# Optimization experiments

Hardware: AMD Instinct MI355X
Metric: run time of the kernel (lower is better)

## Reference

```python
import jax, jax.numpy as jnp
import numpy as np

NUM_EXPERTS = 8


def setup_inputs() -> dict:
    key = jax.random.key(0)
    k1, k2, k3 = jax.random.split(key, 3)
    M, K, E, N, TOPK = 16384, 1024, NUM_EXPERTS, 2048, 2
    local_hidden_states = jax.random.normal(k1, (M, K), dtype=jnp.float32)
    up_weight = jax.random.normal(k2, (E, K, N), dtype=jnp.float32) * 0.02
    full_topk_ids = jax.random.randint(k3, (M, TOPK), 0, E, dtype=jnp.int64)
    return {
        "local_hidden_states": local_hidden_states,
        "up_weight": up_weight,
        "full_topk_ids": full_topk_ids,
    }


def reference(local_hidden_states, up_weight, full_topk_ids):
    # WORLD_SIZE == 1 -> all-gather is the identity; full token set == local shard.
    full_hidden = local_hidden_states                     # [M, K]
    M, K = full_hidden.shape
    E, _, N = up_weight.shape
    topk = full_topk_ids.shape[1]

    # Each token is routed to `topk` experts: replicate rows, flatten routing ids.
    h_rep = jnp.repeat(full_hidden, topk, axis=0)         # [M*topk, K]
    flat_ids = full_topk_ids.reshape(-1)                  # [M*topk]

    # Expert-grouped GEMM: out[p] = h_rep[p] @ up_weight[flat_ids[p]].
    # Loop over the small fixed expert count, masking rows (dense reference
    # for the irregular grouped GEMM; avoids a [M*topk, K, N] weight gather).
    inter = jnp.zeros((M * topk, N), dtype=full_hidden.dtype)
    for e in range(E):
        mask = (flat_ids == e).astype(full_hidden.dtype)[:, None]   # [M*topk, 1]
        inter = inter + (h_rep @ up_weight[e]) * mask                # [M*topk, N]

    # Fused gated SiLU: split the fused gate/up projection in half.
    half = N // 2
    gate, up = inter[:, :half], inter[:, half:]
    return jax.nn.silu(gate) * up                          # [M*topk, N//2]
```

## Files before the change

kernel.cpp:

```cpp
#include <hip/hip_runtime.h>
#include <hip/hip_bf16.h>
#include <stdint.h>

typedef __attribute__((ext_vector_type(4))) float f32x4;
typedef __attribute__((ext_vector_type(8))) short bf16x8;
typedef __attribute__((ext_vector_type(4))) float float4v;

static constexpr int KD    = 1024;
static constexpr int ND    = 2048;
static constexpr int NE    = 8;
static constexpr int MROWS = 16384;
static constexpr int RFLAT = 32768;
static constexpr int OUTN  = 1024;

static constexpr size_t WS_ROWLIST = 1024;
static constexpr size_t WS_HB      = 262144;
static constexpr size_t WS_WT      = 262144 + (size_t)33554432;

__device__ __forceinline__ unsigned short f2bf(float f) {
  uint32_t u = __float_as_uint(f);
  uint32_t r = (u + 0x7FFFu + ((u >> 16) & 1u)) >> 16;
  return (unsigned short)r;
}

__device__ __forceinline__ void gload16(const void* g, void* l) {
  __builtin_amdgcn_global_load_lds(
      (__attribute__((address_space(1))) void*)(void*)g,
      (__attribute__((address_space(3))) void*)l, 16, 0, 0);
}

__global__ void k_detect(const int* __restrict__ ids32, int* __restrict__ wsi) {
  int t = blockIdx.x * 256 + threadIdx.x;
  int i = 2 * t + 1;
  if (i < RFLAT && ids32[i] != 0) atomicOr(&wsi[31], 1);
}

__device__ __forceinline__ int read_id(const int* ids32, int t, int mode) {
  return (mode ? ids32[t] : ids32[2 * t]) & 7;
}

__global__ void k_count(const int* __restrict__ ids, int* __restrict__ wsi) {
  __shared__ int h[8];
  const int tid = threadIdx.x;
  if (tid < 8) h[tid] = 0;
  __syncthreads();
  const int mode = wsi[31];
  const int base = blockIdx.x * 512 + tid;
  atomicAdd(&h[read_id(ids, base, mode)], 1);
  atomicAdd(&h[read_id(ids, base + 256, mode)], 1);
  __syncthreads();
  if (tid < 8 && h[tid]) atomicAdd(&wsi[tid], h[tid]);
}

__global__ void k_scan(int* wsi) {
  if (threadIdx.x == 0) {
    int o = 0, to = 0;
    for (int e = 0; e < NE; ++e) {
      int c = wsi[e];
      wsi[16 + e] = o;
      wsi[8 + e]  = o;
      wsi[40 + e] = to;
      o += c;
      to += (c + 255) / 256;
    }
    wsi[16 + NE] = o;
    wsi[40 + NE] = to;
  }
}

__global__ void k_scatter(const int* __restrict__ ids, int* __restrict__ wsi,
                          int* __restrict__ rowlist) {
  __shared__ int h[8], base[8], c2[8];
  const int tid = threadIdx.x;
  if (tid < 8) { h[tid] = 0; c2[tid] = 0; }
  __syncthreads();
  const int mode = wsi[31];
  const int t = blockIdx.x * 256 + tid;
  const int e = read_id(ids, t, mode);
  atomicAdd(&h[e], 1);
  __syncthreads();
  if (tid < 8 && h[tid]) base[tid] = atomicAdd(&wsi[8 + tid], h[tid]);
  __syncthreads();
  const int r = atomicAdd(&c2[e], 1);
  rowlist[base[e] + r] = t;
}

__global__ void k_cvtH(const float* __restrict__ H, unsigned short* __restrict__ Hb) {
  const int n4 = (MROWS * KD) / 4;
  const int stride = gridDim.x * blockDim.x;
  for (int i = blockIdx.x * blockDim.x + threadIdx.x; i < n4; i += stride) {
    float4v v = ((const float4v*)H)[i];
    ushort4 o;
    o.x = f2bf(v.x); o.y = f2bf(v.y); o.z = f2bf(v.z); o.w = f2bf(v.w);
    ((ushort4*)Hb)[i] = o;
  }
}

__global__ void k_cvtW(const float* __restrict__ W, unsigned short* __restrict__ Wt) {
  __shared__ float tile[64][65];
  const int e  = blockIdx.z;
  const int n0 = blockIdx.x * 64;
  const int k0 = blockIdx.y * 64;
  const int tx = threadIdx.x, ty = threadIdx.y;
  const float* Wp = W + (size_t)e * KD * ND;
  #pragma unroll
  for (int i = ty; i < 64; i += 8)
    tile[i][tx] = Wp[(size_t)(k0 + i) * ND + n0 + tx];
  __syncthreads();
  unsigned short* Wo = Wt + (size_t)e * ND * KD;
  #pragma unroll
  for (int i = ty; i < 64; i += 8)
    Wo[(size_t)(n0 + i) * KD + k0 + tx] = f2bf(tile[tx][i]);
}

__global__ __launch_bounds__(512, 2) void k_gemm(
    const unsigned short* __restrict__ Hb, const unsigned short* __restrict__ Wt,
    const int* __restrict__ wsi, const int* __restrict__ rowlist,
    float* __restrict__ Out) {
  const int bid = blockIdx.x;
  const int xcd = bid & 7;
  const int j   = bid >> 3;
  const int colblk = j & 7;
  const int rt  = xcd + (j >> 3) * 8;
  if (rt >= wsi[48]) return;
  int e = 0;
  #pragma unroll
  for (int q = 1; q < 8; ++q)
    if (rt >= wsi[40 + q]) e = q;
  const int cnt = wsi[e];
  const int tile_base = (rt - wsi[40 + e]) * 256;
  const int tile_cnt = min(256, cnt - tile_base);
  const int off = wsi[16 + e] + tile_base;
  const int c0 = colblk * 128;

  __shared__ char lds[131072];
  __shared__ int s_rows[256];

  const int t = threadIdx.x;
  if (t < 256) s_rows[t] = rowlist[off + min(t, tile_cnt - 1)];
  __syncthreads();

  const int srow = t >> 2;
  const int g16 = ((t & 3) ^ ((t >> 3) & 3)) * 16;
  const char* srcA[2];
  const char* srcB[2];
  #pragma unroll
  for (int u = 0; u < 2; ++u) {
    const int row_a = u * 128 + srow;
    srcA[u] = (const char*)Hb + (size_t)(s_rows[row_a] >> 1) * (KD * 2) + g16;
    const int jb = u * 128 + srow;
    const int wn_s = jb >> 6, r64 = jb & 63;
    const int h_s = r64 >> 4, l_s = r64 & 15;
    const int wcol = (h_s < 2) ? (c0 + wn_s * 32 + h_s * 16 + l_s)
                               : (OUTN + c0 + wn_s * 32 + (h_s - 2) * 16 + l_s);
    srcB[u] = (const char*)Wt + ((size_t)e * ND + wcol) * (KD * 2) + g16;
  }

  const int lane = t & 63, wid = t >> 6;
  const int wm = wid >> 2, wn = wid & 3;
  const int kc = lane >> 4, l15 = lane & 15;

  f32x4 acc[8][4];
  #pragma unroll
  for (int m = 0; m < 8; ++m)
    #pragma unroll
    for (int h = 0; h < 4; ++h)
      acc[m][h] = (f32x4){0.f, 0.f, 0.f, 0.f};

  int aoff[8], boff[4];
  #pragma unroll
  for (int m = 0; m < 8; ++m) {
    const int r = wm * 128 + m * 16 + l15;
    aoff[m] = r * 64 + (kc ^ ((r >> 1) & 3)) * 16;
  }
  #pragma unroll
  for (int h = 0; h < 4; ++h) {
    const int jb = wn * 64 + h * 16 + l15;
    boff[h] = 16384 + jb * 64 + (kc ^ ((jb >> 1) & 3)) * 16;
  }

  auto STAGE = [&](int kt, int b) {
    const int go = kt * 64;
    char* base = lds + b * 32768 + t * 16;
    gload16(srcA[0] + go, base);
    gload16(srcA[1] + go, base + 8192);
    gload16(srcB[0] + go, base + 16384);
    gload16(srcB[1] + go, base + 24576);
  };
  auto COMPUTE = [&](int b) {
    const char* cb = lds + b * 32768;
    bf16x8 af[8], bfv[4];
    #pragma unroll
    for (int m = 0; m < 8; ++m) af[m] = *(const bf16x8*)(cb + aoff[m]);
    #pragma unroll
    for (int h = 0; h < 4; ++h) bfv[h] = *(const bf16x8*)(cb + boff[h]);
    #pragma unroll
    for (int m = 0; m < 8; ++m)
      #pragma unroll
      for (int h = 0; h < 4; ++h)
        acc[m][h] = __builtin_amdgcn_mfma_f32_16x16x32_bf16(af[m], bfv[h], acc[m][h], 0, 0, 0);
  };

  STAGE(0, 0); STAGE(1, 1); STAGE(2, 2);
  asm volatile("s_waitcnt vmcnt(8)\ns_barrier" ::: "memory");

  for (int k = 0; k < 29; ++k) {
    STAGE(k + 3, (k + 3) & 3);
    COMPUTE(k & 3);
    asm volatile("s_waitcnt vmcnt(8)\ns_barrier" ::: "memory");
  }
  COMPUTE(29 & 3);
  asm volatile("s_waitcnt vmcnt(4)\ns_barrier" ::: "memory");
  COMPUTE(30 & 3);
  asm volatile("s_waitcnt vmcnt(0)\ns_barrier" ::: "memory");
  COMPUTE(31 & 3);

  #pragma unroll
  for (int m = 0; m < 8; ++m) {
    const int rbase = wm * 128 + m * 16 + kc * 4;
    #pragma unroll
    for (int i = 0; i < 4; ++i) {
      const int rl = rbase + i;
      if (rl < tile_cnt) {
        const size_t orow = (size_t)s_rows[rl] * OUTN;
        #pragma unroll
        for (int h = 0; h < 2; ++h) {
          float gg = acc[m][h][i];
          float uu = acc[m][h + 2][i];
          float s = gg / (1.0f + __expf(-gg)) * uu;
          Out[orow + c0 + wn * 32 + h * 16 + l15] = s;
        }
      }
    }
  }
}

extern "C" void kernel_launch(void* const* d_in, const int* in_sizes, int n_in,
                              void* d_out, int out_size, void* d_ws, size_t ws_size,
                              hipStream_t stream) {
  const float* H  = (const float*)d_in[0];
  const float* W  = (const float*)d_in[1];
  const int* ids  = (const int*)d_in[2];
  float* Out      = (float*)d_out;
  char* ws        = (char*)d_ws;
  int* wsi        = (int*)ws;
  int* rowlist    = (int*)(ws + WS_ROWLIST);
  unsigned short* Hb = (unsigned short*)(ws + WS_HB);
  unsigned short* Wt = (unsigned short*)(ws + WS_WT);

  hipMemsetAsync(ws, 0, 1024, stream);
  k_detect<<<RFLAT / 2 / 256, 256, 0, stream>>>(ids, wsi);
  k_count<<<RFLAT / 512, 256, 0, stream>>>(ids, wsi);
  k_scan<<<1, 64, 0, stream>>>(wsi);
  k_scatter<<<RFLAT / 256, 256, 0, stream>>>(ids, wsi, rowlist);
  k_cvtH<<<2048, 256, 0, stream>>>(H, Hb);
  k_cvtW<<<dim3(ND / 64, KD / 64, NE), dim3(64, 8), 0, stream>>>(W, Wt);
  k_gemm<<<8 * 17 * 8, 512, 0, stream>>>(Hb, Wt, wsi, rowlist, Out);
}
```

Baseline: 262.8 us.

## Restructure GEMM main loop into double-buffered 128-K tiles with interleaved phases

Replaces the 4-stage, 64-wide K pipeline with a 2-buffer scheme using 128-wide K tiles split into two 64-wide halves. Each iteration interleaves LDS fragment loads, global-to-LDS prefetches of the next tile, and MFMA groups in four phases, raising wave priority during MFMA with s_setprio. The goal is to overlap memory and matrix work at a finer grain, in a style similar to ping-pong scheduling. In exchange it adds many more barriers per iteration and relies on the vmcnt waits being correct for the new load ordering.

```diff
diff --git a/kernel.cpp b/kernel.cpp
--- a/kernel.cpp
+++ b/kernel.cpp
@@ -141,20 +141,17 @@
   __syncthreads();
 
   const int srow = t >> 2;
-  const int g16 = ((t & 3) ^ ((t >> 3) & 3)) * 16;
-  const char* srcA[2];
-  const char* srcB[2];
-  #pragma unroll
-  for (int u = 0; u < 2; ++u) {
-    const int row_a = u * 128 + srow;
-    srcA[u] = (const char*)Hb + (size_t)(s_rows[row_a] >> 1) * (KD * 2) + g16;
-    const int jb = u * 128 + srow;
-    const int wn_s = jb >> 6, r64 = jb & 63;
+  const int coff = ((t & 3) ^ ((t >> 3) & 3)) * 16;
+  const char* sA0 = (const char*)Hb + (size_t)(s_rows[srow] >> 1) * (KD * 2) + coff;
+  const char* sA1 = (const char*)Hb + (size_t)(s_rows[128 + srow] >> 1) * (KD * 2) + coff;
+  auto wcol_of = [&](int jc) {
+    const int wn_s = jc >> 6, r64 = jc & 63;
     const int h_s = r64 >> 4, l_s = r64 & 15;
-    const int wcol = (h_s < 2) ? (c0 + wn_s * 32 + h_s * 16 + l_s)
-                               : (OUTN + c0 + wn_s * 32 + (h_s - 2) * 16 + l_s);
-    srcB[u] = (const char*)Wt + ((size_t)e * ND + wcol) * (KD * 2) + g16;
-  }
+    return (h_s < 2) ? (c0 + wn_s * 32 + h_s * 16 + l_s)
+                     : (OUTN + c0 + wn_s * 32 + (h_s - 2) * 16 + l_s);
+  };
+  const char* sB0 = (const char*)Wt + ((size_t)e * ND + wcol_of(srow)) * (KD * 2) + coff;
+  const char* sB1 = (const char*)Wt + ((size_t)e * ND + wcol_of(128 + srow)) * (KD * 2) + coff;
 
   const int lane = t & 63, wid = t >> 6;
   const int wm = wid >> 2, wn = wid & 3;
@@ -167,53 +164,88 @@
     for (int h = 0; h < 4; ++h)
       acc[m][h] = (f32x4){0.f, 0.f, 0.f, 0.f};
 
-  int aoff[8], boff[4];
-  #pragma unroll
-  for (int m = 0; m < 8; ++m) {
-    const int r = wm * 128 + m * 16 + l15;
-    aoff[m] = r * 64 + (kc ^ ((r >> 1) & 3)) * 16;
-  }
-  #pragma unroll
-  for (int h = 0; h < 4; ++h) {
-    const int jb = wn * 64 + h * 16 + l15;
-    boff[h] = 16384 + jb * 64 + (kc ^ ((jb >> 1) & 3)) * 16;
-  }
-
-  auto STAGE = [&](int kt, int b) {
-    const int go = kt * 64;
-    char* base = lds + b * 32768 + t * 16;
-    gload16(srcA[0] + go, base);
-    gload16(srcA[1] + go, base + 8192);
-    gload16(srcB[0] + go, base + 16384);
-    gload16(srcB[1] + go, base + 24576);
-  };
-  auto COMPUTE = [&](int b) {
-    const char* cb = lds + b * 32768;
-    bf16x8 af[8], bfv[4];
-    #pragma unroll
-    for (int m = 0; m < 8; ++m) af[m] = *(const bf16x8*)(cb + aoff[m]);
-    #pragma unroll
-    for (int h = 0; h < 4; ++h) bfv[h] = *(const bf16x8*)(cb + boff[h]);
-    #pragma unroll
-    for (int m = 0; m < 8; ++m)
+  int aoff[2][8], boff[2][4];
+  #pragma unroll
+  for (int q = 0; q < 2; ++q) {
+    #pragma unroll
+    for (int m = 0; m < 8; ++m) {
+      const int r = wm * 128 + m * 16 + l15;
+      aoff[q][m] = q * 16384 + r * 64 + ((kc ^ ((r >> 1) & 3)) * 16);
+    }
+    #pragma unroll
+    for (int h = 0; h < 4; ++h) {
+      const int jb = wn * 64 + h * 16 + l15;
+      boff[q][h] = 32768 + q * 16384 + jb * 64 + ((kc ^ ((jb >> 1) & 3)) * 16);
+    }
+  }
+
+  auto SA = [&](int kt, int q, char* buf) {
+    const int go = kt * 128 + q * 64;
+    gload16(sA0 + go, buf + q * 16384 + t * 16);
+    gload16(sA1 + go, buf + q * 16384 + 8192 + t * 16);
+  };
+  auto SB = [&](int kt, int q, char* buf) {
+    const int go = kt * 128 + q * 64;
+    gload16(sB0 + go, buf + 32768 + q * 16384 + t * 16);
+    gload16(sB1 + go, buf + 32768 + q * 16384 + 8192 + t * 16);
+  };
+
+  bf16x8 af[4], bfv[4];
+  auto LDA = [&](const char* cb, int q, int mlo) {
+    #pragma unroll
+    for (int m = 0; m < 4; ++m) af[m] = *(const bf16x8*)(cb + aoff[q][mlo + m]);
+  };
+  auto LDB = [&](const char* cb, int q) {
+    #pragma unroll
+    for (int h = 0; h < 4; ++h) bfv[h] = *(const bf16x8*)(cb + boff[q][h]);
+  };
+  auto MM = [&](int mlo) {
+    __builtin_amdgcn_s_setprio(1);
+    #pragma unroll
+    for (int m = 0; m < 4; ++m)
       #pragma unroll
       for (int h = 0; h < 4; ++h)
-        acc[m][h] = __builtin_amdgcn_mfma_f32_16x16x32_bf16(af[m], bfv[h], acc[m][h], 0, 0, 0);
-  };
-
-  STAGE(0, 0); STAGE(1, 1); STAGE(2, 2);
-  asm volatile("s_waitcnt vmcnt(8)\ns_barrier" ::: "memory");
-
-  for (int k = 0; k < 29; ++k) {
-    STAGE(k + 3, (k + 3) & 3);
-    COMPUTE(k & 3);
-    asm volatile("s_waitcnt vmcnt(8)\ns_barrier" ::: "memory");
-  }
-  COMPUTE(29 & 3);
-  asm volatile("s_waitcnt vmcnt(4)\ns_barrier" ::: "memory");
-  COMPUTE(30 & 3);
-  asm volatile("s_waitcnt vmcnt(0)\ns_barrier" ::: "memory");
-  COMPUTE(31 & 3);
+        acc[mlo + m][h] =
+            __builtin_amdgcn_mfma_f32_16x16x32_bf16(af[m], bfv[h], acc[mlo + m][h], 0, 0, 0);
+    __builtin_amdgcn_s_setprio(0);
+  };
+#define GUARD4 asm volatile("s_waitcnt vmcnt(4)" ::: "memory")
+#define GUARD0 asm volatile("s_waitcnt vmcnt(0)" ::: "memory")
+#define BAR __builtin_amdgcn_s_barrier()
+
+  SA(0, 0, lds); SB(0, 0, lds); SA(0, 1, lds); SB(0, 1, lds);
+  GUARD4; BAR;
+
+  for (int k = 0; k < 15; ++k) {
+    const char* cb = lds + (k & 1) * 65536;
+    char* nb = lds + ((k + 1) & 1) * 65536;
+    LDA(cb, 0, 0); LDB(cb, 0);
+    SA(k + 1, 0, nb);
+    BAR; MM(0); BAR;
+    LDA(cb, 0, 4);
+    SB(k + 1, 0, nb);
+    GUARD4; BAR; MM(4); BAR;
+    LDA(cb, 1, 0); LDB(cb, 1);
+    SA(k + 1, 1, nb);
+    BAR; MM(0); BAR;
+    LDA(cb, 1, 4);
+    SB(k + 1, 1, nb);
+    GUARD4; BAR; MM(4); BAR;
+  }
+  {
+    const char* cb = lds + 65536;
+    LDA(cb, 0, 0); LDB(cb, 0);
+    BAR; MM(0); BAR;
+    LDA(cb, 0, 4);
+    GUARD0; BAR; MM(4); BAR;
+    LDA(cb, 1, 0); LDB(cb, 1);
+    BAR; MM(0); BAR;
+    LDA(cb, 1, 4);
+    MM(4);
+  }
+#undef GUARD4
+#undef GUARD0
+#undef BAR
 
   #pragma unroll
   for (int m = 0; m < 8; ++m) {
```

Result: faster. 236.0 us (-10.2%).
